# Optimization experiments

Hardware: AMD Instinct MI355X
Metric: run time of the kernel (lower is better)

Reference implementation:

```python
import jax, jax.numpy as jnp
import numpy as np

DIM = 1024
SEQ_LEN = 2048
NUM_HEAD = 16
HEAD_DIM = 64
B = 4


def setup_inputs() -> dict:
    key = jax.random.key(0)
    ks = jax.random.split(key, 9)
    hd = NUM_HEAD * HEAD_DIM
    s_in = 1.0 / np.sqrt(DIM)
    s_o = 1.0 / np.sqrt(hd)
    return {
        "x": jax.random.normal(ks[0], (B, SEQ_LEN, DIM), dtype=jnp.float32),
        "q_w": jax.random.uniform(ks[1], (hd, DIM), jnp.float32, -s_in, s_in),
        "q_b": jax.random.uniform(ks[2], (hd,), jnp.float32, -s_in, s_in),
        "k_w": jax.random.uniform(ks[3], (hd, DIM), jnp.float32, -s_in, s_in),
        "k_b": jax.random.uniform(ks[4], (hd,), jnp.float32, -s_in, s_in),
        "v_w": jax.random.uniform(ks[5], (hd, DIM), jnp.float32, -s_in, s_in),
        "v_b": jax.random.uniform(ks[6], (hd,), jnp.float32, -s_in, s_in),
        "o_w": jax.random.uniform(ks[7], (DIM, hd), jnp.float32, -s_o, s_o),
        "o_b": jax.random.uniform(ks[8], (DIM,), jnp.float32, -s_o, s_o),
    }


def reference(x, q_w, q_b, k_w, k_b, v_w, v_b, o_w, o_b):
    Bn, T, C = x.shape
    # QKV projections (torch Linear: x @ W^T + b)
    q = (x @ q_w.T + q_b).reshape(Bn, T, NUM_HEAD, HEAD_DIM).transpose(0, 2, 1, 3)
    k = (x @ k_w.T + k_b).reshape(Bn, T, NUM_HEAD, HEAD_DIM).transpose(0, 2, 1, 3)
    v = (x @ v_w.T + v_b).reshape(Bn, T, NUM_HEAD, HEAD_DIM).transpose(0, 2, 1, 3)
    scale = HEAD_DIM ** -0.5
    attn = jnp.einsum("bhqd,bhkd->bhqk", q, k) * scale  # (B,H,T,T)
    causal = jnp.tril(jnp.ones((T, T), dtype=bool))
    attn = jnp.where(causal[None, None, :, :], attn, -jnp.inf)
    p = jax.nn.softmax(attn, axis=-1)  # stable softmax (max-subtracted)
    out = jnp.einsum("bhqk,bhkd->bhqd", p, v)
    out = out.transpose(0, 2, 1, 3).reshape(Bn, T, NUM_HEAD * HEAD_DIM)
    return out @ o_w.T + o_b
```

## Files before the change

### kernel.cpp

```cpp
#include <hip/hip_runtime.h>
#include <stdint.h>

typedef short short8 __attribute__((ext_vector_type(8)));
typedef float f32x4 __attribute__((ext_vector_type(4)));

__device__ __forceinline__ unsigned short f2bf(float f) {
    unsigned int u = __float_as_uint(f);
    u += 0x7fffu + ((u >> 16) & 1u);
    return (unsigned short)(u >> 16);
}

__device__ __forceinline__ void gld_lds16(const unsigned short* g, unsigned short* l) {
    __builtin_amdgcn_global_load_lds((const __attribute__((address_space(1))) unsigned int*)g,
                                     (__attribute__((address_space(3))) unsigned int*)l,
                                     16, 0, 0);
}

#define QSCL 0.18033688011112042f

__global__ __launch_bounds__(256) void cvt_all(const float* __restrict__ x,
                                               const float* __restrict__ qw, const float* __restrict__ kw,
                                               const float* __restrict__ vw, const float* __restrict__ ow,
                                               const float* __restrict__ qb, const float* __restrict__ kb,
                                               const float* __restrict__ vb,
                                               unsigned short* __restrict__ Xb,
                                               unsigned short* __restrict__ Wqkv,
                                               unsigned short* __restrict__ Owb,
                                               float* __restrict__ bqkv) {
    int i = blockIdx.x * 256 + threadIdx.x;
    const float* src; uint2* dst; int j;
    if (i < 2097152)      { src = x;  dst = (uint2*)Xb;                j = i; }
    else if (i < 2359296) { src = qw; dst = (uint2*)Wqkv;              j = i - 2097152; }
    else if (i < 2621440) { src = kw; dst = (uint2*)(Wqkv + 1048576);  j = i - 2359296; }
    else if (i < 2883584) { src = vw; dst = (uint2*)(Wqkv + 2097152);  j = i - 2621440; }
    else if (i < 3145728) { src = ow; dst = (uint2*)Owb;               j = i - 2883584; }
    else {
        int t = i - 3145728;
        const float4* bs = (t < 256) ? (const float4*)qb : (t < 512) ? (const float4*)kb : (const float4*)vb;
        ((float4*)bqkv)[t] = bs[t & 255];
        return;
    }
    float4 v = ((const float4*)src)[j];
    unsigned int lo = (unsigned int)f2bf(v.x) | ((unsigned int)f2bf(v.y) << 16);
    unsigned int hi = (unsigned int)f2bf(v.z) | ((unsigned int)f2bf(v.w) << 16);
    dst[j] = make_uint2(lo, hi);
}

template<int MODE>
__global__ __launch_bounds__(256) void gemm_bt(const unsigned short* __restrict__ A,
                                               const unsigned short* __restrict__ Bm,
                                               const float* __restrict__ bias,
                                               void* __restrict__ C0,
                                               unsigned short* __restrict__ VtOut,
                                               int M, int N, int K)
{
    __shared__ __align__(16) unsigned short As[128 * 64];
    __shared__ __align__(16) unsigned short Bs[128 * 64];
    const int tid  = threadIdx.x;
    const int bm   = blockIdx.x, bn = blockIdx.y;
    const int lane = tid & 63, w = tid >> 6;
    const int wm   = w >> 1, wn = w & 1;
    const int quad = lane >> 4, l15 = lane & 15;

    f32x4 acc[4][4];
#pragma unroll
    for (int mt = 0; mt < 4; mt++)
#pragma unroll
        for (int nt = 0; nt < 4; nt++)
            acc[mt][nt] = (f32x4){0.f, 0.f, 0.f, 0.f};

    const int kTiles = K >> 6;
    for (int kt = 0; kt < kTiles; ++kt) {
        __syncthreads();
#pragma unroll
        for (int i = 0; i < 4; i++) {
            int G  = i * 256 + tid;
            int m  = G >> 3, g = G & 7;
            int gs = g ^ (m & 7);
            int Gb = i * 256 + (w << 6);
            gld_lds16(A  + (size_t)(bm * 128 + m) * K + kt * 64 + gs * 8, &As[Gb * 8]);
            gld_lds16(Bm + (size_t)(bn * 128 + m) * K + kt * 64 + gs * 8, &Bs[Gb * 8]);
        }
        __syncthreads();
#pragma unroll
        for (int ks = 0; ks < 2; ++ks) {
            short8 af[4], bfr[4];
#pragma unroll
            for (int mt = 0; mt < 4; mt++) {
                int m = wm * 64 + mt * 16 + l15;
                af[mt] = *(const short8*)&As[m * 64 + (((ks * 4 + quad) ^ (l15 & 7)) << 3)];
            }
#pragma unroll
            for (int nt = 0; nt < 4; nt++) {
                int n = wn * 64 + nt * 16 + l15;
                bfr[nt] = *(const short8*)&Bs[n * 64 + (((ks * 4 + quad) ^ (l15 & 7)) << 3)];
            }
#pragma unroll
            for (int mt = 0; mt < 4; mt++)
#pragma unroll
                for (int nt = 0; nt < 4; nt++)
                    acc[mt][nt] = __builtin_amdgcn_mfma_f32_16x16x32_bf16(af[mt], bfr[nt], acc[mt][nt], 0, 0, 0);
        }
    }
    const int row0 = bm * 128 + wm * 64, col0 = bn * 128 + wn * 64;
#pragma unroll
    for (int nt = 0; nt < 4; nt++) {
        int col = col0 + nt * 16 + l15;
        float bv = bias[col];
#pragma unroll
        for (int mt = 0; mt < 4; mt++) {
            if (MODE == 1 && col >= 2048) {
                int row = row0 + mt * 16 + quad * 4;
                int b = row >> 11, t = row & 2047;
                ushort4 pk;
                pk.x = f2bf(acc[mt][nt][0] + bv);
                pk.y = f2bf(acc[mt][nt][1] + bv);
                pk.z = f2bf(acc[mt][nt][2] + bv);
                pk.w = f2bf(acc[mt][nt][3] + bv);
                *(ushort4*)(VtOut + (size_t)(b * 1024 + (col - 2048)) * 2048 + t) = pk;
            } else {
#pragma unroll
                for (int r = 0; r < 4; r++) {
                    int row = row0 + mt * 16 + quad * 4 + r;
                    float v = acc[mt][nt][r] + bv;
                    if (MODE == 1) {
                        if (col < 1024) v *= QSCL;
                        ((unsigned short*)C0)[(size_t)row * 2048 + col] = f2bf(v);
                    } else {
                        ((float*)C0)[(size_t)row * N + col] = v;
                    }
                }
            }
        }
    }
}

#define NEG_RAW (-1e30f)
__global__ __launch_bounds__(256) void attn_mfma(const unsigned short* __restrict__ QK,
                                                 const unsigned short* __restrict__ Vt,
                                                 unsigned short* __restrict__ O)
{
    __shared__ __align__(16) unsigned short Kb[2][64 * 64];
    __shared__ __align__(16) unsigned short Vb[2][64 * 64];
    __shared__ __align__(16) unsigned short Ps[4 * 32 * 72];
    const int tid  = threadIdx.x;
    const int lane = tid & 63, w = tid >> 6;
    const int quad = lane >> 4, l15 = lane & 15;
    const int bh   = blockIdx.x;
    const int b    = bh >> 4, h = bh & 15;
    const int qt   = (int)gridDim.y - 1 - (int)blockIdx.y;
    const int qbase = qt * 128 + w * 32;

    const unsigned short* Qp = QK + (size_t)(b * 2048) * 2048 + h * 64;
    const unsigned short* Kp = Qp + 1024;
    const unsigned short* Vp = Vt + (size_t)(bh * 64) * 2048;
    unsigned short* Pw = Ps + w * 32 * 72;

    short8 qf[2][2];
#pragma unroll
    for (int mt = 0; mt < 2; mt++)
#pragma unroll
        for (int kk = 0; kk < 2; kk++)
            qf[mt][kk] = *(const short8*)(Qp + (size_t)(qbase + mt * 16 + l15) * 2048 + kk * 32 + quad * 8);

    short8 ones;
#pragma unroll
    for (int j = 0; j < 8; j++) ones[j] = (short)0x3F80;

    f32x4 oacc[2][4], lacc[2];
#pragma unroll
    for (int mt = 0; mt < 2; mt++) {
        lacc[mt] = (f32x4){0.f, 0.f, 0.f, 0.f};
#pragma unroll
        for (int nt = 0; nt < 4; nt++) oacc[mt][nt] = (f32x4){0.f, 0.f, 0.f, 0.f};
    }

    const int ktend   = 2 * qt + 1;
    const int ktmax_w = (qbase + 31) >> 6;

#pragma unroll
    for (int i = 0; i < 2; i++) {
        int G = i * 256 + tid;
        int r = G >> 3, g = G & 7, gs = g ^ (r & 7);
        int Gb = i * 256 + (w << 6);
        gld_lds16(Kp + (size_t)r * 2048 + gs * 8, &Kb[0][Gb * 8]);
        gld_lds16(Vp + (size_t)r * 2048 + gs * 8, &Vb[0][Gb * 8]);
    }
    __syncthreads();

    for (int kt = 0; kt <= ktend; ++kt) {
        const int cur = kt & 1;
        if (kt < ktend) {
            const unsigned short* Kn = Kp + (size_t)((kt + 1) * 64) * 2048;
            const unsigned short* Vn = Vp + (kt + 1) * 64;
#pragma unroll
            for (int i = 0; i < 2; i++) {
                int G = i * 256 + tid;
                int r = G >> 3, g = G & 7, gs = g ^ (r & 7);
                int Gb = i * 256 + (w << 6);
                gld_lds16(Kn + (size_t)r * 2048 + gs * 8, &Kb[cur ^ 1][Gb * 8]);
                gld_lds16(Vn + (size_t)r * 2048 + gs * 8, &Vb[cur ^ 1][Gb * 8]);
            }
        }
        if (kt <= ktmax_w) {
            const unsigned short* Kc = Kb[cur];
            const unsigned short* Vc = Vb[cur];
            const int kbase = kt * 64;
            const bool diag = (kbase + 63 > qbase);
#pragma unroll
            for (int nt = 0; nt < 4; nt++) {
                short8 kf0, kf1;
                {
                    int key = nt * 16 + l15, sw = key & 7;
                    kf0 = *(const short8*)&Kc[key * 64 + ((quad ^ sw) << 3)];
                    kf1 = *(const short8*)&Kc[key * 64 + (((4 + quad) ^ sw) << 3)];
                }
#pragma unroll
                for (int mt = 0; mt < 2; mt++) {
                    if (diag && kbase + nt * 16 > qbase + mt * 16 + 15) {
                        *(uint2*)&Pw[(mt * 16 + l15) * 72 + nt * 16 + quad * 4] = make_uint2(0u, 0u);
                        continue;
                    }
                    f32x4 sacc = (f32x4){0.f, 0.f, 0.f, 0.f};
                    sacc = __builtin_amdgcn_mfma_f32_16x16x32_bf16(kf0, qf[mt][0], sacc, 0, 0, 0);
                    sacc = __builtin_amdgcn_mfma_f32_16x16x32_bf16(kf1, qf[mt][1], sacc, 0, 0, 0);
                    if (diag) {
                        const int qg = qbase + mt * 16 + l15;
#pragma unroll
                        for (int r = 0; r < 4; r++)
                            if (kbase + nt * 16 + quad * 4 + r > qg) sacc[r] = NEG_RAW;
                    }
                    float p0 = __builtin_exp2f(sacc[0]);
                    float p1 = __builtin_exp2f(sacc[1]);
                    float p2 = __builtin_exp2f(sacc[2]);
                    float p3 = __builtin_exp2f(sacc[3]);
                    unsigned int lo = __builtin_amdgcn_perm(__float_as_uint(p1), __float_as_uint(p0), 0x07060302u);
                    unsigned int hi = __builtin_amdgcn_perm(__float_as_uint(p3), __float_as_uint(p2), 0x07060302u);
                    *(uint2*)&Pw[(mt * 16 + l15) * 72 + nt * 16 + quad * 4] = make_uint2(lo, hi);
                }
            }
#pragma unroll
            for (int kv = 0; kv < 2; kv++) {
                short8 pf0 = *(const short8*)&Pw[l15 * 72 + kv * 32 + quad * 8];
                short8 pf1 = *(const short8*)&Pw[(16 + l15) * 72 + kv * 32 + quad * 8];
                lacc[0] = __builtin_amdgcn_mfma_f32_16x16x32_bf16(ones, pf0, lacc[0], 0, 0, 0);
                lacc[1] = __builtin_amdgcn_mfma_f32_16x16x32_bf16(ones, pf1, lacc[1], 0, 0, 0);
#pragma unroll
                for (int nt = 0; nt < 4; nt++) {
                    int d = nt * 16 + l15;
                    short8 vf = *(const short8*)&Vc[d * 64 + (((kv * 4 + quad) ^ (d & 7)) << 3)];
                    oacc[0][nt] = __builtin_amdgcn_mfma_f32_16x16x32_bf16(vf, pf0, oacc[0][nt], 0, 0, 0);
                    oacc[1][nt] = __builtin_amdgcn_mfma_f32_16x16x32_bf16(vf, pf1, oacc[1][nt], 0, 0, 0);
                }
            }
        }
        __syncthreads();
    }

#pragma unroll
    for (int mt = 0; mt < 2; mt++) {
        const float inv = 1.f / lacc[mt][0];
        unsigned short* op = O + (size_t)(b * 2048 + qbase + mt * 16 + l15) * 1024 + h * 64;
#pragma unroll
        for (int nt = 0; nt < 4; nt++) {
            ushort4 pk;
            pk.x = f2bf(oacc[mt][nt][0] * inv);
            pk.y = f2bf(oacc[mt][nt][1] * inv);
            pk.z = f2bf(oacc[mt][nt][2] * inv);
            pk.w = f2bf(oacc[mt][nt][3] * inv);
            *(ushort4*)(op + nt * 16 + quad * 4) = pk;
        }
    }
}

extern "C" void kernel_launch(void* const* d_in, const int* in_sizes, int n_in,
                              void* d_out, int out_size, void* d_ws, size_t ws_size,
                              hipStream_t stream)
{
    const float* x   = (const float*)d_in[0];
    const float* q_w = (const float*)d_in[1];
    const float* q_b = (const float*)d_in[2];
    const float* k_w = (const float*)d_in[3];
    const float* k_b = (const float*)d_in[4];
    const float* v_w = (const float*)d_in[5];
    const float* v_b = (const float*)d_in[6];
    const float* o_w = (const float*)d_in[7];
    const float* o_b = (const float*)d_in[8];
    float* out = (float*)d_out;

    unsigned short* Xb   = (unsigned short*)d_ws;
    unsigned short* Wqkv = Xb + 8388608;
    unsigned short* Owb  = Wqkv + 3145728;
    float*          bqkv = (float*)(Owb + 1048576);
    unsigned short* QK   = (unsigned short*)(bqkv + 3072);
    unsigned short* Vtg  = QK + 16777216;
    unsigned short* Abf  = Vtg + 8388608;

    cvt_all<<<12291, 256, 0, stream>>>(x, q_w, k_w, v_w, o_w, q_b, k_b, v_b,
                                       Xb, Wqkv, Owb, bqkv);
    gemm_bt<1><<<dim3(64, 24), 256, 0, stream>>>(Xb, Wqkv, bqkv, QK, Vtg, 8192, 3072, 1024);
    attn_mfma<<<dim3(64, 16), 256, 0, stream>>>(QK, Vtg, Abf);
    gemm_bt<0><<<dim3(64, 8), 256, 0, stream>>>(Abf, Owb, o_b, out, nullptr, 8192, 1024, 1024);
}
```

Measured before the change: 269.2 us.

## Enlarge attention query tile and load GEMM B operand directly to registers

The attention kernel now handles 256 queries per block (64 per wave) instead of 128, so each K/V tile staged in LDS is reused across twice as many queries and the grid is halved. The GEMM kernel drops the B shared-memory tile and has each wave load its B fragments straight from global memory into registers. This cuts LDS traffic and LDS footprint. In exchange it raises register pressure, adds uncoalesced global loads for B that are repeated across the two M-waves, and loses some causal load balance with fewer, larger attention blocks.

```diff
diff --git a/kernel.cpp b/kernel.cpp
--- a/kernel.cpp
+++ b/kernel.cpp
@@ -55,7 +55,6 @@
                                                int M, int N, int K)
 {
     __shared__ __align__(16) unsigned short As[128 * 64];
-    __shared__ __align__(16) unsigned short Bs[128 * 64];
     const int tid  = threadIdx.x;
     const int bm   = blockIdx.x, bn = blockIdx.y;
     const int lane = tid & 63, w = tid >> 6;
@@ -78,28 +77,29 @@
             int m  = G >> 3, g = G & 7;
             int gs = g ^ (m & 7);
             int Gb = i * 256 + (w << 6);
-            gld_lds16(A  + (size_t)(bm * 128 + m) * K + kt * 64 + gs * 8, &As[Gb * 8]);
-            gld_lds16(Bm + (size_t)(bn * 128 + m) * K + kt * 64 + gs * 8, &Bs[Gb * 8]);
-        }
+            gld_lds16(A + (size_t)(bm * 128 + m) * K + kt * 64 + gs * 8, &As[Gb * 8]);
+        }
+        short8 bfr[2][4];
+#pragma unroll
+        for (int ks = 0; ks < 2; ks++)
+#pragma unroll
+            for (int nt = 0; nt < 4; nt++)
+                bfr[ks][nt] = *(const short8*)(Bm + (size_t)(bn * 128 + wn * 64 + nt * 16 + l15) * K
+                                               + kt * 64 + ks * 32 + quad * 8);
         __syncthreads();
 #pragma unroll
         for (int ks = 0; ks < 2; ++ks) {
-            short8 af[4], bfr[4];
+            short8 af[4];
 #pragma unroll
             for (int mt = 0; mt < 4; mt++) {
                 int m = wm * 64 + mt * 16 + l15;
                 af[mt] = *(const short8*)&As[m * 64 + (((ks * 4 + quad) ^ (l15 & 7)) << 3)];
             }
 #pragma unroll
-            for (int nt = 0; nt < 4; nt++) {
-                int n = wn * 64 + nt * 16 + l15;
-                bfr[nt] = *(const short8*)&Bs[n * 64 + (((ks * 4 + quad) ^ (l15 & 7)) << 3)];
-            }
-#pragma unroll
             for (int mt = 0; mt < 4; mt++)
 #pragma unroll
                 for (int nt = 0; nt < 4; nt++)
-                    acc[mt][nt] = __builtin_amdgcn_mfma_f32_16x16x32_bf16(af[mt], bfr[nt], acc[mt][nt], 0, 0, 0);
+                    acc[mt][nt] = __builtin_amdgcn_mfma_f32_16x16x32_bf16(af[mt], bfr[ks][nt], acc[mt][nt], 0, 0, 0);
         }
     }
     const int row0 = bm * 128 + wm * 64, col0 = bn * 128 + wn * 64;
@@ -142,23 +142,23 @@
 {
     __shared__ __align__(16) unsigned short Kb[2][64 * 64];
     __shared__ __align__(16) unsigned short Vb[2][64 * 64];
-    __shared__ __align__(16) unsigned short Ps[4 * 32 * 72];
+    __shared__ __align__(16) unsigned short Ps[4 * 64 * 72];
     const int tid  = threadIdx.x;
     const int lane = tid & 63, w = tid >> 6;
     const int quad = lane >> 4, l15 = lane & 15;
     const int bh   = blockIdx.x;
     const int b    = bh >> 4, h = bh & 15;
     const int qt   = (int)gridDim.y - 1 - (int)blockIdx.y;
-    const int qbase = qt * 128 + w * 32;
+    const int qbase = qt * 256 + w * 64;
 
     const unsigned short* Qp = QK + (size_t)(b * 2048) * 2048 + h * 64;
     const unsigned short* Kp = Qp + 1024;
     const unsigned short* Vp = Vt + (size_t)(bh * 64) * 2048;
-    unsigned short* Pw = Ps + w * 32 * 72;
-
-    short8 qf[2][2];
-#pragma unroll
-    for (int mt = 0; mt < 2; mt++)
+    unsigned short* Pw = Ps + w * 64 * 72;
+
+    short8 qf[4][2];
+#pragma unroll
+    for (int mt = 0; mt < 4; mt++)
 #pragma unroll
         for (int kk = 0; kk < 2; kk++)
             qf[mt][kk] = *(const short8*)(Qp + (size_t)(qbase + mt * 16 + l15) * 2048 + kk * 32 + quad * 8);
@@ -167,16 +167,16 @@
 #pragma unroll
     for (int j = 0; j < 8; j++) ones[j] = (short)0x3F80;
 
-    f32x4 oacc[2][4], lacc[2];
-#pragma unroll
-    for (int mt = 0; mt < 2; mt++) {
+    f32x4 oacc[4][4], lacc[4];
+#pragma unroll
+    for (int mt = 0; mt < 4; mt++) {
         lacc[mt] = (f32x4){0.f, 0.f, 0.f, 0.f};
 #pragma unroll
         for (int nt = 0; nt < 4; nt++) oacc[mt][nt] = (f32x4){0.f, 0.f, 0.f, 0.f};
     }
 
-    const int ktend   = 2 * qt + 1;
-    const int ktmax_w = (qbase + 31) >> 6;
+    const int ktend   = 4 * qt + 3;
+    const int ktmax_w = 4 * qt + w;
 
 #pragma unroll
     for (int i = 0; i < 2; i++) {
@@ -216,7 +216,7 @@
                     kf1 = *(const short8*)&Kc[key * 64 + (((4 + quad) ^ sw) << 3)];
                 }
 #pragma unroll
-                for (int mt = 0; mt < 2; mt++) {
+                for (int mt = 0; mt < 4; mt++) {
                     if (diag && kbase + nt * 16 > qbase + mt * 16 + 15) {
                         *(uint2*)&Pw[(mt * 16 + l15) * 72 + nt * 16 + quad * 4] = make_uint2(0u, 0u);
                         continue;
@@ -241,16 +241,19 @@
             }
 #pragma unroll
             for (int kv = 0; kv < 2; kv++) {
-                short8 pf0 = *(const short8*)&Pw[l15 * 72 + kv * 32 + quad * 8];
-                short8 pf1 = *(const short8*)&Pw[(16 + l15) * 72 + kv * 32 + quad * 8];
-                lacc[0] = __builtin_amdgcn_mfma_f32_16x16x32_bf16(ones, pf0, lacc[0], 0, 0, 0);
-                lacc[1] = __builtin_amdgcn_mfma_f32_16x16x32_bf16(ones, pf1, lacc[1], 0, 0, 0);
+                short8 pf[4];
+#pragma unroll
+                for (int mt = 0; mt < 4; mt++) {
+                    pf[mt] = *(const short8*)&Pw[(mt * 16 + l15) * 72 + kv * 32 + quad * 8];
+                    lacc[mt] = __builtin_amdgcn_mfma_f32_16x16x32_bf16(ones, pf[mt], lacc[mt], 0, 0, 0);
+                }
 #pragma unroll
                 for (int nt = 0; nt < 4; nt++) {
                     int d = nt * 16 + l15;
                     short8 vf = *(const short8*)&Vc[d * 64 + (((kv * 4 + quad) ^ (d & 7)) << 3)];
-                    oacc[0][nt] = __builtin_amdgcn_mfma_f32_16x16x32_bf16(vf, pf0, oacc[0][nt], 0, 0, 0);
-                    oacc[1][nt] = __builtin_amdgcn_mfma_f32_16x16x32_bf16(vf, pf1, oacc[1][nt], 0, 0, 0);
+#pragma unroll
+                    for (int mt = 0; mt < 4; mt++)
+                        oacc[mt][nt] = __builtin_amdgcn_mfma_f32_16x16x32_bf16(vf, pf[mt], oacc[mt][nt], 0, 0, 0);
                 }
             }
         }
@@ -258,7 +261,7 @@
     }
 
 #pragma unroll
-    for (int mt = 0; mt < 2; mt++) {
+    for (int mt = 0; mt < 4; mt++) {
         const float inv = 1.f / lacc[mt][0];
         unsigned short* op = O + (size_t)(b * 2048 + qbase + mt * 16 + l15) * 1024 + h * 64;
 #pragma unroll
@@ -299,6 +302,6 @@
     cvt_all<<<12291, 256, 0, stream>>>(x, q_w, k_w, v_w, o_w, q_b, k_b, v_b,
                                        Xb, Wqkv, Owb, bqkv);
     gemm_bt<1><<<dim3(64, 24), 256, 0, stream>>>(Xb, Wqkv, bqkv, QK, Vtg, 8192, 3072, 1024);
-    attn_mfma<<<dim3(64, 16), 256, 0, stream>>>(QK, Vtg, Abf);
+    attn_mfma<<<dim3(64, 8), 256, 0, stream>>>(QK, Vtg, Abf);
     gemm_bt<0><<<dim3(64, 8), 256, 0, stream>>>(Abf, Owb, o_b, out, nullptr, 8192, 1024, 1024);
 }
```

Result: slower. 403.3 us (+49.8%).
